# Kernel optimization log

Measured on AMD Instinct MI355X. Metric: run time of the kernel, lower is better.

The kernel has to match this reference:

```python
import jax, jax.numpy as jnp
import numpy as np

N, DIM1, DIM2 = 4096, 512, 128

def setup_inputs() -> dict:
    key = jax.random.key(0)
    kx, kw = jax.random.split(key)
    X = jax.random.normal(kx, (N, DIM1), dtype=jnp.float32)
    # original module initializes weight to ones; use randn-scaled for a
    # non-degenerate correctness baseline is NOT faithful -> keep ones.
    weight = jnp.ones((DIM2, DIM1, DIM1), dtype=jnp.float32)
    return {"X": X, "weight": weight}

def reference(X, weight):
    # Y[n,k] = x_n^T W_k x_n  == diagonal of X @ W_k @ X^T, computed directly
    # without materializing the NxN matrix.
    XW = jnp.einsum('ni,kij->nkj', X, weight)   # [N, dim2, dim1]
    Y = jnp.einsum('nkj,nj->nk', XW, X)         # [N, dim2]
    return Y
```

## Files before the change

### kernel.cpp

```cpp
#include <hip/hip_runtime.h>

#define D1 512
#define K2 128

typedef __bf16 bf16_t;
typedef bf16_t bf16x8 __attribute__((ext_vector_type(8)));
typedef bf16_t bf16x4 __attribute__((ext_vector_type(4)));
typedef float  f32x4  __attribute__((ext_vector_type(4)));
typedef float  f32x16 __attribute__((ext_vector_type(16)));

#define WBF_OFF 0ull
#define XBF_OFF 67108864ull
#define WS_NEED 71303168ull

__global__ __launch_bounds__(256)
void prep_w(const float* __restrict__ W, bf16_t* __restrict__ Wbf)
{
    const int k  = blockIdx.x >> 4;
    const int is = blockIdx.x & 15;
    const int t  = threadIdx.x;
    __shared__ float lt[16384];
    char* ltb = (char*)lt;
    {
        const int r  = t >> 3;
        const int cb = (t & 7) * 64;
        const float* src = W + ((size_t)k * D1 + is * 32 + r) * D1 + cb;
        const int sw = (r & 15) << 4;
        #pragma unroll
        for (int c = 0; c < 16; ++c) {
            float4 v = *reinterpret_cast<const float4*>(src + c * 4);
            *reinterpret_cast<float4*>(ltb + r * 2048 + (((cb + c * 4) * 4) ^ sw)) = v;
        }
    }
    __syncthreads();
    bf16_t* out = Wbf + ((size_t)k * 16 + is) * 16384;
    #pragma unroll
    for (int p = 0; p < 8; ++p) {
        const int cc = p * 256 + t;
        const int s  = cc >> 6;
        const int l2 = cc & 63;
        const int il = l2 & 31;
        const int jb = s * 16 + (l2 >> 5) * 8;
        const int sw = (il & 15) << 4;
        bf16x8 h;
        #pragma unroll
        for (int e = 0; e < 8; ++e) {
            float v = *reinterpret_cast<const float*>(ltb + il * 2048 + (((jb + e) * 4) ^ sw));
            h[e] = (bf16_t)v;
        }
        *reinterpret_cast<bf16x8*>(out + (size_t)cc * 8) = h;
    }
}

__global__ __launch_bounds__(256)
void prep_x(const float* __restrict__ X, bf16_t* __restrict__ Xbf)
{
    const int nb2 = blockIdx.x >> 2;
    const int jc  = blockIdx.x & 3;
    const int t   = threadIdx.x;
    __shared__ float xt[16384];
    {
        const int nl = t >> 1;
        const int cb = (t & 1) * 64;
        const float* src = X + ((size_t)nb2 * 128 + nl) * D1 + jc * 128 + cb;
        #pragma unroll
        for (int c = 0; c < 16; ++c) {
            float4 v = *reinterpret_cast<const float4*>(src + c * 4);
            *reinterpret_cast<float4*>(&xt[nl * 128 + cb + c * 4]) = v;
        }
    }
    __syncthreads();
    bf16_t* outx = Xbf + ((size_t)nb2 * 4 + jc) * 16384;
    #pragma unroll
    for (int p = 0; p < 8; ++p) {
        const int cc   = p * 256 + t;
        const int n    = cc >> 4;
        const int slot = cc & 15;
        const int j8   = slot ^ (n & 15);
        bf16x8 h;
        #pragma unroll
        for (int e = 0; e < 8; ++e) h[e] = (bf16_t)xt[n * 128 + j8 * 8 + e];
        *reinterpret_cast<bf16x8*>(outx + (size_t)cc * 8) = h;
    }
}

__global__ __launch_bounds__(512, 4)
void tr_main(const bf16_t* __restrict__ Wbf, const bf16_t* __restrict__ Xbf,
             float* __restrict__ Y)
{
    extern __shared__ char smem[];
    float* red = (float*)(smem + 65536);

    const int bid = blockIdx.x;
    const int k   = (bid & 7) + ((bid >> 9) << 3);
    const int nb  = (bid >> 3) & 63;

    const int tid = threadIdx.x;
    const int w   = tid >> 6;
    const int l   = tid & 63;
    const int l31 = l & 31;
    const int lh  = l >> 5;

    {
        const bf16_t* src = Xbf + (size_t)(nb >> 1) * 65536 + (size_t)(nb & 1) * 8192;
        bf16x8 tmp[8];
        #pragma unroll
        for (int jc = 0; jc < 4; ++jc)
            #pragma unroll
            for (int p = 0; p < 2; ++p) {
                const int ci = p * 512 + tid;
                tmp[jc * 2 + p] = *reinterpret_cast<const bf16x8*>(
                    src + (size_t)jc * 16384 + (size_t)ci * 8);
            }
        #pragma unroll
        for (int jc = 0; jc < 4; ++jc)
            #pragma unroll
            for (int p = 0; p < 2; ++p) {
                const int ci = p * 512 + tid;
                *reinterpret_cast<bf16x8*>(smem + jc * 16384 + ci * 16) = tmp[jc * 2 + p];
            }
    }
    __syncthreads();

    const bf16_t* A0 = Wbf + ((size_t)k * 16 + w * 2) * 16384 + (size_t)l * 8;
    const int sw = (l & 15) << 4;

    f32x16 acc[2][2] = {};

    bf16x8 Aq[2][2];
    #pragma unroll
    for (int d = 0; d < 2; ++d) {
        Aq[d][0] = *reinterpret_cast<const bf16x8*>(A0 + (size_t)d * 512);
        Aq[d][1] = *reinterpret_cast<const bf16x8*>(A0 + 16384 + (size_t)d * 512);
    }

    auto bread = [&](bf16x8* dst, int su) {
        const char* base = smem + (su >> 3) * 16384;
        const int ct = ((((su & 7) * 2 + lh) << 4)) ^ sw;
        #pragma unroll
        for (int fn = 0; fn < 2; ++fn)
            dst[fn] = *reinterpret_cast<const bf16x8*>(
                base + (fn * 32 + l31) * 256 + ct);
    };

    bf16x8 B[2][2];
    bread(B[0], 0);

    #pragma unroll
    for (int s = 0; s < 32; ++s) {
        const int qi = s & 1;
        bf16x8 a0 = Aq[qi][0];
        bf16x8 a1 = Aq[qi][1];
        if (s + 2 < 32) {
            Aq[qi][0] = *reinterpret_cast<const bf16x8*>(A0 + (size_t)(s + 2) * 512);
            Aq[qi][1] = *reinterpret_cast<const bf16x8*>(A0 + 16384 + (size_t)(s + 2) * 512);
        }
        if (s < 31) bread(B[(s + 1) & 1], s + 1);
        __builtin_amdgcn_s_setprio(1);
        acc[0][0] = __builtin_amdgcn_mfma_f32_32x32x16_bf16(a0, B[qi][0], acc[0][0], 0, 0, 0);
        acc[0][1] = __builtin_amdgcn_mfma_f32_32x32x16_bf16(a0, B[qi][1], acc[0][1], 0, 0, 0);
        acc[1][0] = __builtin_amdgcn_mfma_f32_32x32x16_bf16(a1, B[qi][0], acc[1][0], 0, 0, 0);
        acc[1][1] = __builtin_amdgcn_mfma_f32_32x32x16_bf16(a1, B[qi][1], acc[1][1], 0, 0, 0);
        __builtin_amdgcn_s_setprio(0);
    }

    float yp[2] = {0.f, 0.f};
    #pragma unroll
    for (int mi = 0; mi < 2; ++mi) {
        const int st32 = w * 2 + mi;
        const char* base = smem + (st32 >> 2) * 16384;
        #pragma unroll
        for (int rq = 0; rq < 4; ++rq) {
            const int slot = (st32 * 4 + rq) & 15;
            #pragma unroll
            for (int fn = 0; fn < 2; ++fn) {
                const int n = fn * 32 + l31;
                bf16x4 xv = *reinterpret_cast<const bf16x4*>(
                    base + n * 256 + ((slot ^ (n & 15)) << 4) + lh * 8);
                #pragma unroll
                for (int q = 0; q < 4; ++q)
                    yp[fn] += acc[mi][fn][rq * 4 + q] * (float)xv[q];
            }
        }
    }
    #pragma unroll
    for (int fn = 0; fn < 2; ++fn) {
        float v = yp[fn];
        v += __shfl_down(v, 32);
        if (lh == 0) red[w * 64 + fn * 32 + l31] = v;
    }
    __syncthreads();
    if (tid < 64) {
        float s2 = 0.f;
        #pragma unroll
        for (int w2 = 0; w2 < 8; ++w2) s2 += red[w2 * 64 + tid];
        Y[((size_t)nb * 64 + tid) * K2 + k] = s2;
    }
}

__global__ __launch_bounds__(512, 2)
void tensor_reduction_kernel(const float* __restrict__ X,
                             const float* __restrict__ W,
                             float* __restrict__ Y)
{
    const int bid = blockIdx.x;
    const int xcd = bid & 7;
    const int rr_ = bid >> 3;
    const int kk  = xcd + 8 * (rr_ >> 4);
    const int nb  = (rr_ & 15) * 256;

    const int tid = threadIdx.x;
    const int wv  = tid >> 6;
    const int ln  = tid & 63;
    const int lg  = ln >> 4;
    const int lr  = ln & 15;

    __shared__ __align__(16) bf16_t Xs[256 * 64];
    __shared__ __align__(16) bf16_t Ws[2][64 * 64];

    bf16x8 afrag[2][16];
    {
        const int srow = tid >> 4;
        const int sj4  = (tid & 15) * 4;
        #pragma unroll
        for (int c = 0; c < 8; ++c) {
            #pragma unroll
            for (int p = 0; p < 8; ++p) {
                const int row = p * 32 + srow;
                float4 v = *reinterpret_cast<const float4*>(
                    X + (size_t)(nb + row) * D1 + c * 64 + sj4);
                bf16x4 h = { (bf16_t)v.x, (bf16_t)v.y, (bf16_t)v.z, (bf16_t)v.w };
                const int byte = row * 128 + ((sj4 * 2) ^ ((row & 7) << 4));
                *reinterpret_cast<bf16x4*>((char*)Xs + byte) = h;
            }
            __syncthreads();
            #pragma unroll
            for (int m = 0; m < 2; ++m) {
                #pragma unroll
                for (int ks = 0; ks < 2; ++ks) {
                    const int row  = wv * 32 + m * 16 + lr;
                    const int byte = row * 128 + ((ks * 64 + lg * 16) ^ ((row & 7) << 4));
                    afrag[m][2 * c + ks] =
                        *reinterpret_cast<const bf16x8*>((const char*)Xs + byte);
                }
            }
            __syncthreads();
        }
    }

    const float* Wk  = W + (size_t)kk * D1 * D1;
    const int irow = tid >> 3;
    const int j8   = (tid & 7) * 8;

    float ypart[2][4] = {{0.f,0.f,0.f,0.f},{0.f,0.f,0.f,0.f}};

    {
        const float* src = Wk + (size_t)irow * D1 + j8;
        float4 u0 = *reinterpret_cast<const float4*>(src);
        float4 u1 = *reinterpret_cast<const float4*>(src + 4);
        bf16x8 h = { (bf16_t)u0.x,(bf16_t)u0.y,(bf16_t)u0.z,(bf16_t)u0.w,
                     (bf16_t)u1.x,(bf16_t)u1.y,(bf16_t)u1.z,(bf16_t)u1.w };
        const int byte = irow * 128 + ((j8 * 2) ^ ((irow & 7) << 4));
        *reinterpret_cast<bf16x8*>((char*)Ws[0] + byte) = h;
    }
    __syncthreads();

    for (int it = 0; it < 8; ++it) {
        f32x4 acc[2][4] = {};
        #pragma unroll
        for (int jcc = 0; jcc < 8; ++jcc) {
            const int tI  = it * 8 + jcc;
            const int cur = tI & 1;
            float4 u0, u1;
            const bool pf = (tI < 63);
            if (pf) {
                const int nit = (tI + 1) >> 3, njc = (tI + 1) & 7;
                const float* src = Wk + (size_t)(nit * 64 + irow) * D1 + njc * 64 + j8;
                u0 = *reinterpret_cast<const float4*>(src);
                u1 = *reinterpret_cast<const float4*>(src + 4);
            }
            #pragma unroll
            for (int ks = 0; ks < 2; ++ks) {
                bf16x8 bfr[4];
                #pragma unroll
                for (int f = 0; f < 4; ++f) {
                    const int ir   = f * 16 + lr;
                    const int byte = ir * 128 + ((ks * 64 + lg * 16) ^ ((ir & 7) << 4));
                    bfr[f] = *reinterpret_cast<const bf16x8*>((const char*)Ws[cur] + byte);
                }
                #pragma unroll
                for (int m = 0; m < 2; ++m)
                    #pragma unroll
                    for (int f = 0; f < 4; ++f)
                        acc[m][f] = __builtin_amdgcn_mfma_f32_16x16x32_bf16(
                            afrag[m][2 * jcc + ks], bfr[f], acc[m][f], 0, 0, 0);
            }
            if (pf) {
                bf16x8 h = { (bf16_t)u0.x,(bf16_t)u0.y,(bf16_t)u0.z,(bf16_t)u0.w,
                             (bf16_t)u1.x,(bf16_t)u1.y,(bf16_t)u1.z,(bf16_t)u1.w };
                const int byte = irow * 128 + ((j8 * 2) ^ ((irow & 7) << 4));
                *reinterpret_cast<bf16x8*>((char*)Ws[cur ^ 1] + byte) = h;
            }
            __syncthreads();
        }
        #pragma unroll
        for (int m = 0; m < 2; ++m) {
            #pragma unroll
            for (int f = 0; f < 4; ++f) {
                const int col = it * 64 + f * 16 + lr;
                #pragma unroll
                for (int q = 0; q < 4; ++q) {
                    const int grow = nb + wv * 32 + m * 16 + lg * 4 + q;
                    ypart[m][q] += acc[m][f][q] * X[(size_t)grow * D1 + col];
                }
            }
        }
    }

    #pragma unroll
    for (int m = 0; m < 2; ++m) {
        #pragma unroll
        for (int q = 0; q < 4; ++q) {
            float v = ypart[m][q];
            v += __shfl_xor(v, 1, 64);
            v += __shfl_xor(v, 2, 64);
            v += __shfl_xor(v, 4, 64);
            v += __shfl_xor(v, 8, 64);
            if (lr == 0) {
                const int grow = nb + wv * 32 + m * 16 + lg * 4 + q;
                Y[(size_t)grow * K2 + kk] = v;
            }
        }
    }
}

extern "C" void kernel_launch(void* const* d_in, const int* in_sizes, int n_in,
                              void* d_out, int out_size, void* d_ws, size_t ws_size,
                              hipStream_t stream)
{
    const float* X = (const float*)d_in[0];
    const float* W = (const float*)d_in[1];
    float* Y = (float*)d_out;

    if (d_ws != nullptr && ws_size >= WS_NEED) {
        bf16_t* Wbf = (bf16_t*)((char*)d_ws + WBF_OFF);
        bf16_t* Xbf = (bf16_t*)((char*)d_ws + XBF_OFF);
        prep_w<<<2048, 256, 0, stream>>>(W, Wbf);
        prep_x<<<128, 256, 0, stream>>>(X, Xbf);
        (void)hipFuncSetAttribute((const void*)tr_main,
                                  hipFuncAttributeMaxDynamicSharedMemorySize, 67584);
        tr_main<<<8192, 512, 67584, stream>>>(Wbf, Xbf, Y);
    } else {
        tensor_reduction_kernel<<<2048, 512, 0, stream>>>(X, W, Y);
    }
}
```

Baseline: 278.8 us.

## Reshape tr_main wave tiling to 4 W tiles by 1 X tile per wave

Each wave now computes four 32-row W tiles against a single 32-row X tile, instead of a 2x2 tile block. This halves the LDS reads of X per MFMA and simplifies the epilogue, which reduces over 4 partial rows instead of 8. In exchange, each W slice is now fetched from global memory by two waves per block instead of one. The W prefetch is also shortened from two steps ahead to a single load issued after the MFMAs, so less global latency is hidden.

New measurement: 354.2 us. +27.0%, slower.

```diff
diff --git a/kernel.cpp b/kernel.cpp
--- a/kernel.cpp
+++ b/kernel.cpp
@@ -97,9 +97,12 @@
 
     const int tid = threadIdx.x;
     const int w   = tid >> 6;
+    const int ip  = w & 3;
+    const int h   = w >> 2;
     const int l   = tid & 63;
     const int l31 = l & 31;
     const int lh  = l >> 5;
+    const int sw  = (l & 15) << 4;
 
     {
         const bf16_t* src = Xbf + (size_t)(nb >> 1) * 65536 + (size_t)(nb & 1) * 8192;
@@ -122,78 +125,68 @@
     }
     __syncthreads();
 
-    const bf16_t* A0 = Wbf + ((size_t)k * 16 + w * 2) * 16384 + (size_t)l * 8;
-    const int sw = (l & 15) << 4;
-
-    f32x16 acc[2][2] = {};
-
-    bf16x8 Aq[2][2];
-    #pragma unroll
-    for (int d = 0; d < 2; ++d) {
-        Aq[d][0] = *reinterpret_cast<const bf16x8*>(A0 + (size_t)d * 512);
-        Aq[d][1] = *reinterpret_cast<const bf16x8*>(A0 + 16384 + (size_t)d * 512);
-    }
+    const bf16_t* A0 = Wbf + ((size_t)k * 16 + ip * 4) * 16384 + (size_t)l * 8;
+
+    f32x16 acc[4] = {};
+
+    bf16x8 A[4], B[2];
+    #pragma unroll
+    for (int mi = 0; mi < 4; ++mi)
+        A[mi] = *reinterpret_cast<const bf16x8*>(A0 + (size_t)mi * 16384);
 
     auto bread = [&](bf16x8* dst, int su) {
         const char* base = smem + (su >> 3) * 16384;
         const int ct = ((((su & 7) * 2 + lh) << 4)) ^ sw;
-        #pragma unroll
-        for (int fn = 0; fn < 2; ++fn)
-            dst[fn] = *reinterpret_cast<const bf16x8*>(
-                base + (fn * 32 + l31) * 256 + ct);
+        *dst = *reinterpret_cast<const bf16x8*>(
+            base + (h * 32 + l31) * 256 + ct);
     };
 
-    bf16x8 B[2][2];
-    bread(B[0], 0);
+    bread(&B[0], 0);
 
     #pragma unroll
     for (int s = 0; s < 32; ++s) {
         const int qi = s & 1;
-        bf16x8 a0 = Aq[qi][0];
-        bf16x8 a1 = Aq[qi][1];
-        if (s + 2 < 32) {
-            Aq[qi][0] = *reinterpret_cast<const bf16x8*>(A0 + (size_t)(s + 2) * 512);
-            Aq[qi][1] = *reinterpret_cast<const bf16x8*>(A0 + 16384 + (size_t)(s + 2) * 512);
-        }
-        if (s < 31) bread(B[(s + 1) & 1], s + 1);
+        if (s + 1 < 32) bread(&B[qi ^ 1], s + 1);
         __builtin_amdgcn_s_setprio(1);
-        acc[0][0] = __builtin_amdgcn_mfma_f32_32x32x16_bf16(a0, B[qi][0], acc[0][0], 0, 0, 0);
-        acc[0][1] = __builtin_amdgcn_mfma_f32_32x32x16_bf16(a0, B[qi][1], acc[0][1], 0, 0, 0);
-        acc[1][0] = __builtin_amdgcn_mfma_f32_32x32x16_bf16(a1, B[qi][0], acc[1][0], 0, 0, 0);
-        acc[1][1] = __builtin_amdgcn_mfma_f32_32x32x16_bf16(a1, B[qi][1], acc[1][1], 0, 0, 0);
+        acc[0] = __builtin_amdgcn_mfma_f32_32x32x16_bf16(A[0], B[qi], acc[0], 0, 0, 0);
+        acc[1] = __builtin_amdgcn_mfma_f32_32x32x16_bf16(A[1], B[qi], acc[1], 0, 0, 0);
+        acc[2] = __builtin_amdgcn_mfma_f32_32x32x16_bf16(A[2], B[qi], acc[2], 0, 0, 0);
+        acc[3] = __builtin_amdgcn_mfma_f32_32x32x16_bf16(A[3], B[qi], acc[3], 0, 0, 0);
         __builtin_amdgcn_s_setprio(0);
-    }
-
-    float yp[2] = {0.f, 0.f};
-    #pragma unroll
-    for (int mi = 0; mi < 2; ++mi) {
-        const int st32 = w * 2 + mi;
+        if (s + 1 < 32) {
+            #pragma unroll
+            for (int mi = 0; mi < 4; ++mi)
+                A[mi] = *reinterpret_cast<const bf16x8*>(
+                    A0 + (size_t)mi * 16384 + (size_t)(s + 1) * 512);
+        }
+    }
+
+    float yp = 0.f;
+    #pragma unroll
+    for (int mi = 0; mi < 4; ++mi) {
+        const int st32 = ip * 4 + mi;
         const char* base = smem + (st32 >> 2) * 16384;
         #pragma unroll
         for (int rq = 0; rq < 4; ++rq) {
             const int slot = (st32 * 4 + rq) & 15;
-            #pragma unroll
-            for (int fn = 0; fn < 2; ++fn) {
-                const int n = fn * 32 + l31;
-                bf16x4 xv = *reinterpret_cast<const bf16x4*>(
-                    base + n * 256 + ((slot ^ (n & 15)) << 4) + lh * 8);
-                #pragma unroll
-                for (int q = 0; q < 4; ++q)
-                    yp[fn] += acc[mi][fn][rq * 4 + q] * (float)xv[q];
-            }
-        }
-    }
-    #pragma unroll
-    for (int fn = 0; fn < 2; ++fn) {
-        float v = yp[fn];
+            const int n = h * 32 + l31;
+            bf16x4 xv = *reinterpret_cast<const bf16x4*>(
+                base + n * 256 + ((slot ^ (n & 15)) << 4) + lh * 8);
+            #pragma unroll
+            for (int q = 0; q < 4; ++q)
+                yp += acc[mi][rq * 4 + q] * (float)xv[q];
+        }
+    }
+    {
+        float v = yp;
         v += __shfl_down(v, 32);
-        if (lh == 0) red[w * 64 + fn * 32 + l31] = v;
+        if (lh == 0) red[ip * 64 + h * 32 + l31] = v;
     }
     __syncthreads();
     if (tid < 64) {
         float s2 = 0.f;
         #pragma unroll
-        for (int w2 = 0; w2 < 8; ++w2) s2 += red[w2 * 64 + tid];
+        for (int p = 0; p < 4; ++p) s2 += red[p * 64 + tid];
         Y[((size_t)nb * 64 + tid) * K2 + k] = s2;
     }
 }
```
